# Kernel optimization log

Measured on AMD Instinct MI355X. Metric: run time of the kernel, lower is better.

The kernel has to match this reference:

```python
import jax, jax.numpy as jnp
import numpy as np

B, T, D, H = 4, 2048, 1024, 16
DK = D // H

def setup_inputs() -> dict:
    key = jax.random.key(0)
    ks = jax.random.split(key, 9)
    s = 0.02
    return {
        "x": jax.random.normal(ks[0], (B, T, D), dtype=jnp.float32),
        "Wq": jax.random.normal(ks[1], (D, D), dtype=jnp.float32) * s,
        "bq": jnp.zeros((D,), dtype=jnp.float32),
        "Wk": jax.random.normal(ks[2], (D, D), dtype=jnp.float32) * s,
        "bk": jnp.zeros((D,), dtype=jnp.float32),
        "Wv": jax.random.normal(ks[3], (D, D), dtype=jnp.float32) * s,
        "bv": jnp.zeros((D,), dtype=jnp.float32),
        "Wo": jax.random.normal(ks[4], (D, D), dtype=jnp.float32) * s,
        "bo": jnp.zeros((D,), dtype=jnp.float32),
    }

def reference(x, Wq, bq, Wk, bk, Wv, bv, Wo, bo):
    b, t, c = x.shape
    # projections -> [B, H, T, DK]
    def split_heads(y):
        return y.reshape(b, t, H, DK).transpose(0, 2, 1, 3)
    q = split_heads(x @ Wq.T + bq)
    k = split_heads(x @ Wk.T + bk)
    v = split_heads(x @ Wv.T + bv)
    scale = 1.0 / jnp.sqrt(jnp.asarray(DK, dtype=x.dtype))
    scores = jnp.einsum("bhqd,bhkd->bhqk", q, k) * scale  # [B,H,T,T]
    causal = jnp.tril(jnp.ones((t, t), dtype=bool))
    scores = jnp.where(causal, scores, jnp.asarray(-jnp.inf, dtype=scores.dtype))
    attn = jax.nn.softmax(scores, axis=-1)
    out = jnp.einsum("bhqk,bhkd->bhqd", attn, v)  # [B,H,T,DK]
    out = out.transpose(0, 2, 1, 3).reshape(b, t, c)
    return out @ Wo.T + bo
```

## Files before the change

kernel.cpp:

```cpp
#include <hip/hip_runtime.h>
#include <hip/hip_bf16.h>

#define DEV __device__ __forceinline__

typedef unsigned short u16;
typedef unsigned int u32;
typedef __attribute__((ext_vector_type(4))) float f32x4;
typedef __attribute__((ext_vector_type(16))) float f32x16;
typedef __attribute__((ext_vector_type(8))) __bf16 bf16x8;
typedef __attribute__((ext_vector_type(8))) u16 u16x8;
typedef __attribute__((ext_vector_type(4))) u16 u16x4;
typedef __attribute__((ext_vector_type(4))) u32 u32x4;

#define CSCALE 0.18033688011112042f

DEV u16 f2bf(float f) {
    u32 u = __builtin_bit_cast(u32, f);
    u32 r = (u + 0x7fffu + ((u >> 16) & 1u)) >> 16;
    return (u16)r;
}

DEV u16 f2bf_fast(float f) {
    u32 u = __builtin_bit_cast(u32, f);
    return (u16)((u + 0x8000u) >> 16);
}

DEV float fastrcp(float x) {
#if __has_builtin(__builtin_amdgcn_rcpf)
    return __builtin_amdgcn_rcpf(x);
#else
    return 1.0f / x;
#endif
}

DEV u32 cvtpk_bf16(float lo, float hi) {
    u32 r;
    asm("v_cvt_pk_bf16_f32 %0, %1, %2" : "=v"(r) : "v"(lo), "v"(hi));
    return r;
}

DEV void plswap(u32& a, u32& b) {
    asm volatile("v_permlane32_swap_b32 %0, %1" : "+v"(a), "+v"(b));
}

DEV void gload_lds16(const void* g, void* l) {
    void* gg = const_cast<void*>(g);
    __builtin_amdgcn_global_load_lds(
        (const __attribute__((address_space(1))) void*)gg,
        (__attribute__((address_space(3))) void*)l,
        16, 0, 0);
}

DEV f32x16 mfma32(bf16x8 a, bf16x8 b, f32x16 c) {
    return __builtin_amdgcn_mfma_f32_32x32x16_bf16(a, b, c, 0, 0, 0);
}

__global__ void cvt_f32_bf16(const float* __restrict__ in, u16* __restrict__ out,
                             int n4, float scale) {
    int i = blockIdx.x * blockDim.x + threadIdx.x;
    if (i < n4) {
        float4 v = ((const float4*)in)[i];
        u16x4 o;
        o[0] = f2bf(v.x * scale); o[1] = f2bf(v.y * scale);
        o[2] = f2bf(v.z * scale); o[3] = f2bf(v.w * scale);
        ((u16x4*)out)[i] = o;
    }
}

__global__ void build_bias(const float* __restrict__ bq, const float* __restrict__ bk,
                           const float* __restrict__ bv, float* __restrict__ o) {
    int i = blockIdx.x * blockDim.x + threadIdx.x;
    if (i < 3072) {
        float v;
        if (i < 1024) v = bq[i] * CSCALE;
        else if (i < 2048) v = bk[i - 1024];
        else v = bv[i - 2048];
        o[i] = v;
    }
}

template<int F32OUT>
__global__ __launch_bounds__(256) void gemm_bt(
    const u16* __restrict__ A, const u16* __restrict__ B,
    const float* __restrict__ bias, void* __restrict__ Cv,
    int K, int ldc, int bnPerXcd)
{
    __shared__ u16 As[128 * 64];
    __shared__ u16 Bs[128 * 64];
    const int t = threadIdx.x;
    const int lane = t & 63;
    const int w = t >> 6;
    const int wm = w >> 1, wn = w & 1;
    const int id = (int)blockIdx.x;
    const int xcd = id & 7, r = id >> 3;
    const int bm = (r / bnPerXcd) * 128;
    const int bn = (xcd * bnPerXcd + r % bnPerXcd) * 128;
    const int lr = lane & 15;
    const int lg = lane >> 4;
    const int swz = (lr & 7) << 4;

    f32x4 acc[4][4] = {};

    for (int k0 = 0; k0 < K; k0 += 64) {
        #pragma unroll
        for (int i = 0; i < 4; ++i) {
            int idx = t + i * 256;
            int row = idx >> 3;
            int gsrc = (idx & 7) ^ (row & 7);
            gload_lds16((const char*)A + ((size_t)(bm + row) * K + k0 + gsrc * 8) * 2,
                        (char*)As + idx * 16);
            gload_lds16((const char*)B + ((size_t)(bn + row) * K + k0 + gsrc * 8) * 2,
                        (char*)Bs + idx * 16);
        }
        __syncthreads();
        #pragma unroll
        for (int kk = 0; kk < 2; ++kk) {
            bf16x8 af[4], bfr[4];
            #pragma unroll
            for (int m = 0; m < 4; ++m)
                af[m] = *(const bf16x8*)((const char*)As + (wm * 64 + m * 16 + lr) * 128 +
                                         ((kk * 64 + lg * 16) ^ swz));
            #pragma unroll
            for (int n = 0; n < 4; ++n)
                bfr[n] = *(const bf16x8*)((const char*)Bs + (wn * 64 + n * 16 + lr) * 128 +
                                          ((kk * 64 + lg * 16) ^ swz));
            #pragma unroll
            for (int m = 0; m < 4; ++m)
                #pragma unroll
                for (int n = 0; n < 4; ++n)
                    acc[m][n] = __builtin_amdgcn_mfma_f32_16x16x32_bf16(af[m], bfr[n], acc[m][n], 0, 0, 0);
        }
        __syncthreads();
    }

    #pragma unroll
    for (int n = 0; n < 4; ++n) {
        int col = bn + wn * 64 + n * 16 + lr;
        float bv = bias[col];
        #pragma unroll
        for (int m = 0; m < 4; ++m) {
            int row0 = bm + wm * 64 + m * 16 + lg * 4;
            #pragma unroll
            for (int r2 = 0; r2 < 4; ++r2) {
                float v = acc[m][n][r2] + bv;
                size_t idx = (size_t)(row0 + r2) * ldc + col;
                if (F32OUT) ((float*)Cv)[idx] = v;
                else        ((u16*)Cv)[idx] = f2bf(v);
            }
        }
    }
}

__global__ __launch_bounds__(256, 2) void attn_fwd(
    const u16* __restrict__ QKV, u16* __restrict__ Om)
{
    constexpr int T = 2048, LD = 3072, DO = 1024;
    constexpr int PSTR = 72;
    constexpr float NEG = -3.0e38f;

    __shared__ __align__(16) u16 Ks[2][64 * 64];
    __shared__ __align__(16) u16 Vt[2][64 * PSTR];

    const int t = threadIdx.x, lane = t & 63, w = t >> 6;
    const int ql = lane & 31, hi = lane >> 5;

    const int id = (int)blockIdx.x;
    const int slot = id >> 6;
    const int bh = (id & 7) * 8 + ((id >> 3) & 7);
    const int q0 = (15 - slot) * 128;
    const int b = bh >> 4, h = bh & 15;
    const size_t rowbase = (size_t)b * T * LD + h * 64;
    const u16* Qm = QKV + rowbase;
    const u16* Km = QKV + rowbase + 1024;
    const u16* Vm = QKV + rowbase + 2048;
    const int nt = q0 / 64 + 2;

    const int qg = q0 + w * 32 + ql;
    const int qmax = q0 + w * 32 + 31;

    bf16x8 qf[4];
    {
        const u16* qp = Qm + (size_t)qg * LD + hi * 8;
        #pragma unroll
        for (int s = 0; s < 4; ++s) qf[s] = *(const bf16x8*)(qp + s * 16);
    }

    f32x16 oa[2] = {};
    float lsum = 0.f;

    const int krow = t >> 3, kslot = t & 7;
    const u16* kCur = Km + (size_t)krow * LD + 8 * (kslot ^ (krow & 7));
    const int kv2 = (t & 31) * 2, dd = (t >> 5) * 8;
    const u16* vCur = Vm + (size_t)kv2 * LD + dd;
    u16x8 vva, vvb;

    auto stageK = [&](int buf) {
        u16* dst = (u16*)Ks + buf * 4096 + t * 8;
        gload_lds16(kCur, dst);
        gload_lds16(kCur + 32 * LD, dst + 2048);
        kCur += 64 * LD;
    };
    auto loadV = [&]() {
        vva = *(const u16x8*)vCur;
        vvb = *(const u16x8*)(vCur + LD);
        vCur += 64 * LD;
    };
    auto writeVt = [&](int buf) {
        u32* vd = (u32*)((u16*)Vt + buf * (64 * PSTR) + dd * PSTR + kv2);
        #pragma unroll
        for (int j = 0; j < 8; ++j)
            vd[j * (PSTR / 2)] = (u32)vva[j] | ((u32)vvb[j] << 16);
    };

    stageK(0);
    loadV();
    writeVt(0);

    for (int it0 = 0; it0 < nt; it0 += 2) {
        #pragma unroll
        for (int half = 0; half < 2; ++half) {
            const int BUF = half;
            const int it = it0 + half;
            const int kv0 = it * 64;
            __syncthreads();

            const bool more = (it + 1 < nt);
            if (more) { stageK(BUF ^ 1); loadV(); }

            const bool a0  = kv0 <= qmax;
            const bool a0h = kv0 + 32 <= qmax;

            f32x16 sa[2] = {};
            __builtin_amdgcn_s_setprio(1);
            #pragma unroll
            for (int n = 0; n < 2; ++n) {
                if (!(n ? a0h : a0)) continue;
                const int row = n * 32 + ql;
                const int swz = (row & 7) << 4;
                #pragma unroll
                for (int s = 0; s < 4; ++s) {
                    bf16x8 kf = *(const bf16x8*)((const char*)Ks + BUF * 8192 + row * 128 +
                                                 ((((s << 1) | hi) << 4) ^ swz));
                    sa[n] = mfma32(kf, qf[s], sa[n]);
                }
            }
            __builtin_amdgcn_s_setprio(0);

            u32x4 pw[2][2];
            if (a0) {
                float rs = 0.f;
                #pragma unroll
                for (int n = 0; n < 2; ++n) {
                    if (n == 1 && !a0h) continue;
                    if (kv0 + n * 32 + 31 > q0 + w * 32) {
                        #pragma unroll
                        for (int r = 0; r < 16; ++r) {
                            int kvg = kv0 + n * 32 + (r & 3) + 8 * (r >> 2) + 4 * hi;
                            if (kvg > qg) sa[n][r] = NEG;
                        }
                    }
                    float pv[16];
                    #pragma unroll
                    for (int r = 0; r < 16; ++r)
                        pv[r] = __builtin_exp2f(sa[n][r]);
                    float s8[8];
                    #pragma unroll
                    for (int r = 0; r < 8; ++r) s8[r] = pv[r] + pv[r + 8];
                    rs += ((s8[0] + s8[4]) + (s8[1] + s8[5])) + ((s8[2] + s8[6]) + (s8[3] + s8[7]));
                    #pragma unroll
                    for (int s = 0; s < 2; ++s) {
                        u32 u0 = cvtpk_bf16(pv[8 * s + 0], pv[8 * s + 1]);
                        u32 u1 = cvtpk_bf16(pv[8 * s + 2], pv[8 * s + 3]);
                        u32 u2 = cvtpk_bf16(pv[8 * s + 4], pv[8 * s + 5]);
                        u32 u3 = cvtpk_bf16(pv[8 * s + 6], pv[8 * s + 7]);
                        plswap(u0, u2);
                        plswap(u1, u3);
                        pw[n][s] = u32x4{u0, u1, u2, u3};
                    }
                }
                rs += __shfl_xor(rs, 32);
                lsum += rs;
            }

            __builtin_amdgcn_s_setprio(1);
            #pragma unroll
            for (int dt = 0; dt < 2; ++dt) {
                const int vrow = dt * 32 + ql;
                #pragma unroll
                for (int n = 0; n < 2; ++n) {
                    if (!(n ? a0h : a0)) continue;
                    #pragma unroll
                    for (int s = 0; s < 2; ++s) {
                        bf16x8 vf = *(const bf16x8*)((const u16*)Vt + BUF * (64 * PSTR) +
                                                     vrow * PSTR + n * 32 + s * 16 + hi * 8);
                        oa[dt] = mfma32(vf, __builtin_bit_cast(bf16x8, pw[n][s]), oa[dt]);
                    }
                }
            }
            __builtin_amdgcn_s_setprio(0);

            if (more) writeVt(BUF ^ 1);
        }
    }

    __syncthreads();
    u16* ot = ((u16*)Vt) + w * (32 * PSTR);
    const float inv = fastrcp(lsum);
    #pragma unroll
    for (int dt = 0; dt < 2; ++dt)
        #pragma unroll
        for (int r = 0; r < 16; ++r) {
            int d = dt * 32 + (r & 3) + 8 * (r >> 2) + 4 * hi;
            ot[ql * PSTR + d] = f2bf_fast(oa[dt][r] * inv);
        }
    const int lq = lane >> 1, hv = lane & 1;
    const size_t obase = (size_t)b * T * DO + h * 64;
    const u16* src = ot + lq * PSTR + hv * 32;
    u16* dst = Om + obase + (size_t)(q0 + w * 32 + lq) * DO + hv * 32;
    #pragma unroll
    for (int seg = 0; seg < 4; ++seg)
        *(u16x8*)(dst + seg * 8) = *(const u16x8*)(src + seg * 8);
}

extern "C" void kernel_launch(void* const* d_in, const int* in_sizes, int n_in,
                              void* d_out, int out_size, void* d_ws, size_t ws_size,
                              hipStream_t stream)
{
    const float* x  = (const float*)d_in[0];
    const float* Wq = (const float*)d_in[1];
    const float* bq = (const float*)d_in[2];
    const float* Wk = (const float*)d_in[3];
    const float* bk = (const float*)d_in[4];
    const float* Wv = (const float*)d_in[5];
    const float* bv = (const float*)d_in[6];
    const float* Wo = (const float*)d_in[7];
    const float* bo = (const float*)d_in[8];

    constexpr int T = 2048, D = 1024;
    constexpr size_t MT = (size_t)4 * T;

    const size_t NEED = (size_t)74 << 20;
    if (ws_size < NEED) return;

    char* ws = (char*)d_ws;
    u16* xb    = (u16*)(ws);
    u16* Ob    = (u16*)(ws);
    u16* Wqkvb = (u16*)(ws + ((size_t)16 << 20));
    u16* Wob   = (u16*)(ws + ((size_t)22 << 20));
    u16* QKVb  = (u16*)(ws + ((size_t)24 << 20));
    float* bqkv = (float*)(ws + ((size_t)72 << 20));

    int nx4 = (int)(MT * D / 4);
    cvt_f32_bf16<<<(nx4 + 255) / 256, 256, 0, stream>>>(x, xb, nx4, 1.0f);
    int nw4 = D * D / 4;
    cvt_f32_bf16<<<(nw4 + 255) / 256, 256, 0, stream>>>(Wq, Wqkvb, nw4, CSCALE);
    cvt_f32_bf16<<<(nw4 + 255) / 256, 256, 0, stream>>>(Wk, Wqkvb + (size_t)D * D, nw4, 1.0f);
    cvt_f32_bf16<<<(nw4 + 255) / 256, 256, 0, stream>>>(Wv, Wqkvb + (size_t)2 * D * D, nw4, 1.0f);
    cvt_f32_bf16<<<(nw4 + 255) / 256, 256, 0, stream>>>(Wo, Wob, nw4, 1.0f);
    build_bias<<<12, 256, 0, stream>>>(bq, bk, bv, bqkv);

    gemm_bt<0><<<dim3(1536), 256, 0, stream>>>(xb, Wqkvb, bqkv, QKVb, D, 3072, 3);

    attn_fwd<<<dim3(1024), 256, 0, stream>>>(QKVb, Ob);

    gemm_bt<1><<<dim3(512), 256, 0, stream>>>(Ob, Wob, bo, d_out, D, 1024, 1);
}
```

Measured before the change: 175.7 us.

## Add 256x256-tile 8-wave QKV GEMM with interleaved prefetch and LDS-staged epilogue

Replaces the QKV projection GEMM with a new kernel that uses 512 threads and 256x256 output tiles, double-buffering 64-wide K slices into swizzled LDS. Global-to-LDS loads for the next slice are spread across the MFMA phases, and wave priority is raised around MFMA bursts. The epilogue stages bf16 results through LDS so global stores are coalesced 16-byte writes. Larger tiles cut global reloads of A and B, but the grid shrinks to 384 blocks and LDS use is 128KB per block, which may limit occupancy.

Measured after the change: 180.9 us. +3.0%, slower.

```diff
diff --git a/kernel.cpp b/kernel.cpp
--- a/kernel.cpp
+++ b/kernel.cpp
@@ -151,6 +151,134 @@
     }
 }
 
+__global__ __launch_bounds__(512, 2) void gemm_qkv8(
+    const u16* __restrict__ A, const u16* __restrict__ B,
+    const float* __restrict__ bias, u16* __restrict__ C,
+    int K, int ldc, int ncols)
+{
+    constexpr int TBUF = 256 * 64;
+    __shared__ __align__(16) u16 lds[4 * TBUF >> 1 << 1];
+    u16* As = lds;
+    u16* Bs = lds + 2 * TBUF;
+
+    const int t = threadIdx.x;
+    const int lane = t & 63, w = t >> 6;
+    const int wm = w >> 2, wn = w & 3;
+    const int lr = lane & 15, lg = lane >> 4;
+    const int swz = (lr & 7) << 4;
+
+    const int id = (int)blockIdx.x;
+    const int bm = (id / ncols) * 256;
+    const int bn = (id % ncols) * 256;
+    const int NT = K >> 6;
+
+    const u16* aSrc[4];
+    const u16* bSrc[4];
+    #pragma unroll
+    for (int i = 0; i < 4; ++i) {
+        int idx = t + i * 512, row = idx >> 3, g = idx & 7;
+        aSrc[i] = A + (size_t)(bm + row) * K + ((g ^ (row & 7)) * 8);
+        bSrc[i] = B + (size_t)(bn + row) * K + ((g ^ (row & 7)) * 8);
+    }
+
+    f32x4 acc[8][4] = {};
+
+    #pragma unroll
+    for (int i = 0; i < 4; ++i) {
+        gload_lds16(aSrc[i], As + (t + i * 512) * 8);
+        gload_lds16(bSrc[i], Bs + (t + i * 512) * 8);
+        aSrc[i] += 64; bSrc[i] += 64;
+    }
+    asm volatile("s_waitcnt vmcnt(0)" ::: "memory");
+    __builtin_amdgcn_s_barrier();
+
+    for (int kt0 = 0; kt0 < NT; kt0 += 2) {
+        #pragma unroll
+        for (int hh = 0; hh < 2; ++hh) {
+            const int BUF = hh;
+            const int kt = kt0 + hh;
+            const bool more = (kt + 1 < NT);
+            const char* Ab = (const char*)(As + BUF * TBUF);
+            const char* Bb = (const char*)(Bs + BUF * TBUF);
+            u16* An = As + (BUF ^ 1) * TBUF;
+            u16* Bn = Bs + (BUF ^ 1) * TBUF;
+
+            bf16x8 bfr[2][4];
+            #pragma unroll
+            for (int p = 0; p < 4; ++p) {
+                if (p == 0) {
+                    #pragma unroll
+                    for (int kk = 0; kk < 2; ++kk)
+                        #pragma unroll
+                        for (int n = 0; n < 4; ++n)
+                            bfr[kk][n] = *(const bf16x8*)(Bb +
+                                (wn * 64 + n * 16 + lr) * 128 + ((kk * 64 + lg * 16) ^ swz));
+                }
+                bf16x8 af[2][2];
+                #pragma unroll
+                for (int kk = 0; kk < 2; ++kk)
+                    #pragma unroll
+                    for (int m2 = 0; m2 < 2; ++m2)
+                        af[kk][m2] = *(const bf16x8*)(Ab +
+                            (wm * 128 + (p * 2 + m2) * 16 + lr) * 128 + ((kk * 64 + lg * 16) ^ swz));
+                if (more && p < 2) {
+                    #pragma unroll
+                    for (int i = p * 2; i < p * 2 + 2; ++i) {
+                        gload_lds16(aSrc[i], An + (t + i * 512) * 8);
+                        gload_lds16(bSrc[i], Bn + (t + i * 512) * 8);
+                        aSrc[i] += 64; bSrc[i] += 64;
+                    }
+                }
+                __builtin_amdgcn_s_barrier();
+                asm volatile("s_waitcnt lgkmcnt(0)" ::: "memory");
+                __builtin_amdgcn_s_setprio(1);
+                #pragma unroll
+                for (int kk = 0; kk < 2; ++kk)
+                    #pragma unroll
+                    for (int m2 = 0; m2 < 2; ++m2)
+                        #pragma unroll
+                        for (int n = 0; n < 4; ++n)
+                            acc[p * 2 + m2][n] = __builtin_amdgcn_mfma_f32_16x16x32_bf16(
+                                af[kk][m2], bfr[kk][n], acc[p * 2 + m2][n], 0, 0, 0);
+                __builtin_amdgcn_s_setprio(0);
+                if (p == 3 && more)
+                    asm volatile("s_waitcnt vmcnt(0)" ::: "memory");
+                __builtin_amdgcn_s_barrier();
+            }
+        }
+    }
+
+    const int wcol = bn + wn * 64;
+    float bv[4];
+    #pragma unroll
+    for (int n = 0; n < 4; ++n) bv[n] = bias[wcol + n * 16 + lr];
+    u16* ot = lds + w * (64 * 72);
+    const int rowR = lane >> 1, segC = (lane & 1) * 32;
+    #pragma unroll
+    for (int pass = 0; pass < 2; ++pass) {
+        if (pass) { asm volatile("s_waitcnt lgkmcnt(0)" ::: "memory"); __builtin_amdgcn_s_barrier(); }
+        #pragma unroll
+        for (int mm = 0; mm < 4; ++mm)
+            #pragma unroll
+            for (int n = 0; n < 4; ++n)
+                #pragma unroll
+                for (int r = 0; r < 4; ++r)
+                    ot[(mm * 16 + lg * 4 + r) * 72 + n * 16 + lr] =
+                        f2bf(acc[pass * 4 + mm][n][r] + bv[n]);
+        asm volatile("s_waitcnt lgkmcnt(0)" ::: "memory");
+        #pragma unroll
+        for (int half = 0; half < 2; ++half) {
+            int row_l = rowR + half * 32;
+            int grow = bm + wm * 128 + pass * 64 + row_l;
+            const u16* src = ot + row_l * 72 + segC;
+            u16* dst = C + (size_t)grow * ldc + wcol + segC;
+            #pragma unroll
+            for (int s2 = 0; s2 < 4; ++s2)
+                *(u16x8*)(dst + s2 * 8) = *(const u16x8*)(src + s2 * 8);
+        }
+    }
+}
+
 __global__ __launch_bounds__(256, 2) void attn_fwd(
     const u16* __restrict__ QKV, u16* __restrict__ Om)
 {
@@ -359,7 +487,7 @@
     cvt_f32_bf16<<<(nw4 + 255) / 256, 256, 0, stream>>>(Wo, Wob, nw4, 1.0f);
     build_bias<<<12, 256, 0, stream>>>(bq, bk, bv, bqkv);
 
-    gemm_bt<0><<<dim3(1536), 256, 0, stream>>>(xb, Wqkvb, bqkv, QKVb, D, 3072, 3);
+    gemm_qkv8<<<dim3(384), 512, 0, stream>>>(xb, Wqkvb, bqkv, QKVb, D, 3072, 12);
 
     attn_fwd<<<dim3(1024), 256, 0, stream>>>(QKVb, Ob);
 
```
